# Optimization experiments

Hardware: AMD Instinct MI355X
Metric: run time of the kernel (lower is better)

The kernel has to match this reference:

```python
import jax, jax.numpy as jnp
import numpy as np

DIM = 768
HEADS = 12
HID = 3072  # mlp_ratio * dim
BATCH = 8
FRAMES = 16
GRID = 14
NTOK = GRID * GRID
LN_EPS = 1e-5
EPS = 1e-6


def setup_inputs() -> dict:
    key = jax.random.key(0)
    ks = jax.random.split(key, 8)
    w = lambda k, shape: jax.random.normal(k, shape, jnp.float32) * 0.02
    return {
        "x": jax.random.normal(ks[0], (BATCH * FRAMES, NTOK, DIM), jnp.float32),
        "ln1_w": jnp.ones((DIM,), jnp.float32),
        "ln1_b": jnp.zeros((DIM,), jnp.float32),
        "qkv_w": w(ks[1], (3 * DIM, DIM)),
        "proj_w": w(ks[2], (DIM, DIM)),
        "proj_b": jnp.zeros((DIM,), jnp.float32),
        "ln2_w": jnp.ones((DIM,), jnp.float32),
        "ln2_b": jnp.zeros((DIM,), jnp.float32),
        "fc1_w": w(ks[3], (HID, DIM)),
        "fc1_b": jnp.zeros((HID,), jnp.float32),
        "dw_w": w(ks[4], (HID, 1, 3, 3)),
        "dw_b": jnp.zeros((HID,), jnp.float32),
        "fc2_w": w(ks[5], (DIM, HID)),
        "fc2_b": jnp.zeros((DIM,), jnp.float32),
        "H": GRID,
        "W": GRID,
        "num_frames": FRAMES,
    }


def _layernorm(x, w, b):
    mu = jnp.mean(x, axis=-1, keepdims=True)
    var = jnp.mean(jnp.square(x - mu), axis=-1, keepdims=True)
    return (x - mu) * jax.lax.rsqrt(var + LN_EPS) * w + b


def _joint_ts_attention(xn, qkv_w, proj_w, proj_b, num_frames):
    # xn: (b*f, n, c)
    Bt, n, C = xn.shape
    h = HEADS
    e = C // h
    scale = e ** (-0.5)
    qkv = jnp.einsum('bnc,dc->bnd', xn, qkv_w).reshape(Bt, n, 3, h, e)
    q, k, v = qkv[:, :, 0], qkv[:, :, 1], qkv[:, :, 2]
    # ReLU feature map + scale offset
    q_ = jax.nn.relu(q) + scale
    k_ = jax.nn.relu(k) + scale
    b = Bt // num_frames
    m = num_frames * n  # joint time-space sequence length
    q_ = q_.reshape(b, m, h, e)
    k_ = k_.reshape(b, m, h, e)
    v_ = v.reshape(b, m, h, e)
    # kv_: (b, h, e, e)
    kv = jnp.einsum('bnhe,bnhd->bhed', k_, v_)
    k_sum = jnp.sum(k_, axis=1)  # (b, h, e)
    z = 1.0 / (jnp.einsum('bnhe,bhe->bnh', q_, k_sum) + EPS)  # (b, m, h)
    out = jnp.einsum('bnhe,bhed->bnhd', q_, kv) * z[..., None]  # (b, m, h, e)
    out = out.reshape(Bt, n, C)
    return jnp.einsum('bnc,dc->bnd', out, proj_w) + proj_b


def _dwconv(x, w, b, H, W):
    # x: (B, N, C) -> NCHW depthwise 3x3, pad 1
    Bn, n, c = x.shape
    xi = jnp.transpose(x, (0, 2, 1)).reshape(Bn, c, H, W)
    y = jax.lax.conv_general_dilated(
        xi, w, window_strides=(1, 1), padding=((1, 1), (1, 1)),
        dimension_numbers=('NCHW', 'OIHW', 'NCHW'), feature_group_count=c)
    y = y + b[None, :, None, None]
    return jnp.transpose(y.reshape(Bn, c, n), (0, 2, 1))


def reference(x, ln1_w, ln1_b, qkv_w, proj_w, proj_b, ln2_w, ln2_b,
              fc1_w, fc1_b, dw_w, dw_b, fc2_w, fc2_b, H, W, num_frames):
    # x = x + attn(norm1(x), num_frames)
    x = x + _joint_ts_attention(_layernorm(x, ln1_w, ln1_b), qkv_w, proj_w, proj_b, num_frames)
    # x = x + mlp(norm2(x), H, W)
    xn = _layernorm(x, ln2_w, ln2_b)
    hdn = jnp.einsum('bnc,hc->bnh', xn, fc1_w) + fc1_b
    hdn = _dwconv(hdn, dw_w, dw_b, H, W)
    hdn = jax.nn.gelu(hdn, approximate=False)
    out = jnp.einsum('bnh,ch->bnc', hdn, fc2_w) + fc2_b
    return x + out
```

## Files before the change

kernel.cpp:

```cpp
#include <hip/hip_runtime.h>

typedef unsigned short u16;
typedef unsigned int u32;

typedef __bf16 bf16x8 __attribute__((ext_vector_type(8)));
typedef float f32x4 __attribute__((ext_vector_type(4)));

#define DIM 768
#define HID 3072
#define NTOK 196
#define BT 128
#define NTOKENS (BT * NTOK)
#define MJ 3136
#define HEADS 12

#define QB_ELE ((size_t)NTOKENS * 768)

#define SZ_WB   ((size_t)(2304*768 + 768*768 + 3072*768 + 768*3072) * 2)
#define SZ_XN   ((size_t)NTOKENS * DIM * 2)
#define SZ_QKV  ((size_t)NTOKENS * 2304 * 2)
#define SZ_X2   ((size_t)NTOKENS * DIM * 4)
#define SZ_HDN  ((size_t)NTOKENS * HID * 2)
#define SZ_KV   ((size_t)96 * 4096 * 4)
#define SZ_KS   ((size_t)96 * 64 * 4)
#define WS_NEED (SZ_WB + SZ_XN + SZ_QKV + SZ_X2 + SZ_HDN + SZ_KV + SZ_KS)

static void* g_buf = nullptr;

__device__ __forceinline__ float b2f(u16 u) {
  union { u32 i; float f; } x; x.i = ((u32)u) << 16; return x.f;
}
__device__ __forceinline__ u16 f2b(float f) {
  u32 x = __float_as_uint(f);
  return (u16)((x + 0x7fffu + ((x >> 16) & 1u)) >> 16);
}

__device__ __forceinline__ void gload_lds16(const u16* g, u16* l) {
  __builtin_amdgcn_global_load_lds(
      (const __attribute__((address_space(1))) u32*)g,
      (__attribute__((address_space(3))) u32*)l, 16, 0, 0);
}

__global__ __launch_bounds__(256) void cvt_f32_bf16(const float* __restrict__ in,
    u16* __restrict__ out, int n4)
{
  int i = blockIdx.x * 256 + threadIdx.x;
  if (i < n4) {
    float4 f = ((const float4*)in)[i];
    ushort4 r;
    r.x = f2b(f.x); r.y = f2b(f.y); r.z = f2b(f.z); r.w = f2b(f.w);
    ((ushort4*)out)[i] = r;
  }
}

__global__ __launch_bounds__(256) void zero_f32(float* __restrict__ p, int n) {
  int i = blockIdx.x * 256 + threadIdx.x;
  if (i < n) p[i] = 0.0f;
}

__global__ __launch_bounds__(256) void ln_kernel(const float* __restrict__ xin,
    const float* __restrict__ w, const float* __restrict__ b, u16* __restrict__ out)
{
  const int token = blockIdx.x * 4 + (threadIdx.x >> 6);
  const int lane = threadIdx.x & 63;
  float v[12];
  const float* x = xin + (size_t)token * DIM;
#pragma unroll
  for (int c = 0; c < 3; ++c) {
    float4 f = *(const float4*)(x + c * 256 + lane * 4);
    v[c*4+0] = f.x; v[c*4+1] = f.y; v[c*4+2] = f.z; v[c*4+3] = f.w;
  }
  float s = 0.f, sq = 0.f;
#pragma unroll
  for (int i = 0; i < 12; ++i) { s += v[i]; sq += v[i] * v[i]; }
#pragma unroll
  for (int off = 32; off > 0; off >>= 1) {
    s += __shfl_xor(s, off, 64);
    sq += __shfl_xor(sq, off, 64);
  }
  const float mean = s * (1.0f / 768.0f);
  const float var = sq * (1.0f / 768.0f) - mean * mean;
  const float rstd = rsqrtf(var + 1e-5f);
  u16* o = out + (size_t)token * DIM;
#pragma unroll
  for (int c = 0; c < 3; ++c) {
    float4 wv = *(const float4*)(w + c * 256 + lane * 4);
    float4 bv = *(const float4*)(b + c * 256 + lane * 4);
    ushort4 r;
    r.x = f2b((v[c*4+0] - mean) * rstd * wv.x + bv.x);
    r.y = f2b((v[c*4+1] - mean) * rstd * wv.y + bv.y);
    r.z = f2b((v[c*4+2] - mean) * rstd * wv.z + bv.z);
    r.w = f2b((v[c*4+3] - mean) * rstd * wv.w + bv.w);
    *(ushort4*)(o + c * 256 + lane * 4) = r;
  }
}

template<int MODE, int NXT, int NN, int KK>
__global__ __launch_bounds__(512, 2) void gemm8(
    const u16* __restrict__ A, const u16* __restrict__ W,
    const float* __restrict__ bias, const float* __restrict__ res,
    void* __restrict__ out)
{
  extern __shared__ char smem[];
  u16* As = (u16*)smem;
  u16* Bs = (u16*)(smem + 65536);

  const int t = threadIdx.x;
  const int l = t & 63;
  const int w = t >> 6;
  const int wm = w >> 2;
  const int wn = w & 3;

  constexpr int TOTAL = 98 * NXT;
  constexpr int Q8 = TOTAL >> 3;
  constexpr int R8 = TOTAL & 7;
  const int orig = blockIdx.x;
  const int xcd = orig & 7;
  const int idx = orig >> 3;
  const int wg = (xcd < R8) ? (xcd * (Q8 + 1) + idx)
                            : (R8 * (Q8 + 1) + (xcd - R8) * Q8 + idx);
  const int m0 = (wg / NXT) * 256;
  const int n0 = (wg % NXT) * 256;

  const int srow = w * 16 + (l >> 3);
  const int scol = ((l & 7) ^ (l >> 3)) * 8;
  const u16* gA = A + (size_t)(m0 + srow) * KK + scol;
  const u16* gB = W + (size_t)(n0 + srow) * KK + scol;
  u16* lA = As + w * 1024;
  u16* lB = Bs + w * 1024;

#define STAGE_A(bb, h, kt) do { \
    const u16* g_ = gA + (size_t)(h) * 128 * KK + (size_t)(kt) * 64; \
    u16* l_ = lA + (bb) * 16384 + (h) * 8192; \
    gload_lds16(g_, l_); \
    gload_lds16(g_ + (size_t)8 * KK, l_ + 512); } while (0)
#define STAGE_B(bb, h, kt) do { \
    const u16* g_ = gB + (size_t)(h) * 128 * KK + (size_t)(kt) * 64; \
    u16* l_ = lB + (bb) * 16384 + (h) * 8192; \
    gload_lds16(g_, l_); \
    gload_lds16(g_ + (size_t)8 * KK, l_ + 512); } while (0)

  const int lm = l & 15;
  const int qq = l >> 4;
  const int acol = (qq << 4) ^ ((l & 7) << 4);
  const int abase = (wm * 128 + lm) * 128 + acol;
  const int bbase = (wn * 64 + lm) * 128 + acol;

  f32x4 acc[8][4];
#pragma unroll
  for (int mi = 0; mi < 8; ++mi)
#pragma unroll
    for (int ni = 0; ni < 4; ++ni) acc[mi][ni] = (f32x4){0.f, 0.f, 0.f, 0.f};

  constexpr int NT = KK / 64;

  STAGE_A(0, 0, 0); STAGE_A(0, 1, 0); STAGE_B(0, 0, 0); STAGE_B(0, 1, 0);
  STAGE_A(1, 0, 1); STAGE_A(1, 1, 1);
  asm volatile("s_waitcnt vmcnt(4)" ::: "memory");
  __builtin_amdgcn_s_barrier();

  for (int ti = 0; ti < NT; ++ti) {
    const int cb = ti & 1, nb = cb ^ 1;
    const char* Ac = (const char*)As + cb * 32768;
    const char* Bc = (const char*)Bs + cb * 32768;
    bf16x8 a0[4][2], a1[4][2], b01[2][2], b23[2][2];

#pragma unroll
    for (int mi = 0; mi < 4; ++mi) {
      const int off = abase + mi * 2048;
      a0[mi][0] = *(const bf16x8*)(Ac + off);
      a0[mi][1] = *(const bf16x8*)(Ac + (off ^ 64));
    }
#pragma unroll
    for (int ni = 0; ni < 2; ++ni) {
      const int off = bbase + ni * 2048;
      b01[ni][0] = *(const bf16x8*)(Bc + off);
      b01[ni][1] = *(const bf16x8*)(Bc + (off ^ 64));
    }
    if (ti + 1 < NT) STAGE_B(nb, 0, ti + 1);
    __builtin_amdgcn_s_setprio(1);
#pragma unroll
    for (int mi = 0; mi < 4; ++mi)
#pragma unroll
      for (int ni = 0; ni < 2; ++ni) {
        acc[mi][ni] = __builtin_amdgcn_mfma_f32_16x16x32_bf16(a0[mi][0], b01[ni][0], acc[mi][ni], 0, 0, 0);
        acc[mi][ni] = __builtin_amdgcn_mfma_f32_16x16x32_bf16(a0[mi][1], b01[ni][1], acc[mi][ni], 0, 0, 0);
      }
    __builtin_amdgcn_s_setprio(0);

#pragma unroll
    for (int ni = 0; ni < 2; ++ni) {
      const int off = bbase + (ni + 2) * 2048;
      b23[ni][0] = *(const bf16x8*)(Bc + off);
      b23[ni][1] = *(const bf16x8*)(Bc + (off ^ 64));
    }
    if (ti + 1 < NT) STAGE_B(nb, 1, ti + 1);
    __builtin_amdgcn_s_setprio(1);
#pragma unroll
    for (int mi = 0; mi < 4; ++mi)
#pragma unroll
      for (int ni = 0; ni < 2; ++ni) {
        acc[mi][ni + 2] = __builtin_amdgcn_mfma_f32_16x16x32_bf16(a0[mi][0], b23[ni][0], acc[mi][ni + 2], 0, 0, 0);
        acc[mi][ni + 2] = __builtin_amdgcn_mfma_f32_16x16x32_bf16(a0[mi][1], b23[ni][1], acc[mi][ni + 2], 0, 0, 0);
      }
    __builtin_amdgcn_s_setprio(0);

#pragma unroll
    for (int mi = 0; mi < 4; ++mi) {
      const int off = abase + 8192 + mi * 2048;
      a1[mi][0] = *(const bf16x8*)(Ac + off);
      a1[mi][1] = *(const bf16x8*)(Ac + (off ^ 64));
    }
    __builtin_amdgcn_s_setprio(1);
#pragma unroll
    for (int mi = 0; mi < 4; ++mi)
#pragma unroll
      for (int ni = 0; ni < 2; ++ni) {
        acc[mi + 4][ni + 2] = __builtin_amdgcn_mfma_f32_16x16x32_bf16(a1[mi][0], b23[ni][0], acc[mi + 4][ni + 2], 0, 0, 0);
        acc[mi + 4][ni + 2] = __builtin_amdgcn_mfma_f32_16x16x32_bf16(a1[mi][1], b23[ni][1], acc[mi + 4][ni + 2], 0, 0, 0);
      }
    __builtin_amdgcn_s_setprio(0);

    asm volatile("s_waitcnt lgkmcnt(0)" ::: "memory");
    __builtin_amdgcn_s_barrier();

    if (ti + 2 < NT) { STAGE_A(cb, 0, ti + 2); STAGE_A(cb, 1, ti + 2); }

    __builtin_amdgcn_s_setprio(1);
#pragma unroll
    for (int mi = 0; mi < 4; ++mi)
#pragma unroll
      for (int ni = 0; ni < 2; ++ni) {
        acc[mi + 4][ni] = __builtin_amdgcn_mfma_f32_16x16x32_bf16(a1[mi][0], b01[ni][0], acc[mi + 4][ni], 0, 0, 0);
        acc[mi + 4][ni] = __builtin_amdgcn_mfma_f32_16x16x32_bf16(a1[mi][1], b01[ni][1], acc[mi + 4][ni], 0, 0, 0);
      }
    __builtin_amdgcn_s_setprio(0);

    if (ti + 2 < NT) {
      asm volatile("s_waitcnt vmcnt(4)" ::: "memory");
    } else {
      asm volatile("s_waitcnt vmcnt(0)" ::: "memory");
    }
    __builtin_amdgcn_s_barrier();
  }
#undef STAGE_A
#undef STAGE_B

#pragma unroll
  for (int mi = 0; mi < 8; ++mi) {
    const int rbase = m0 + wm * 128 + mi * 16 + qq * 4;
    const int b = rbase / 3136;
    const int mj = rbase - b * 3136;
#pragma unroll
    for (int ni = 0; ni < 4; ++ni) {
      const int col = n0 + wn * 64 + ni * 16 + lm;
      if (MODE == 0) {
        if (col < 768) {
#pragma unroll
          for (int r = 0; r < 4; ++r) {
            float v = fmaxf(acc[mi][ni][r], 0.0f) + 0.125f;
            ((u16*)out)[(size_t)(rbase + r) * 768 + col] = f2b(v);
          }
        } else {
          const bool isV = (col >= 1536);
          const int cc = col - (isV ? 1536 : 768);
          const int h = cc >> 6, e = cc & 63;
          ushort4 pk;
          float v0 = acc[mi][ni][0], v1 = acc[mi][ni][1];
          float v2 = acc[mi][ni][2], v3 = acc[mi][ni][3];
          if (!isV) {
            v0 = fmaxf(v0, 0.0f) + 0.125f; v1 = fmaxf(v1, 0.0f) + 0.125f;
            v2 = fmaxf(v2, 0.0f) + 0.125f; v3 = fmaxf(v3, 0.0f) + 0.125f;
          }
          pk.x = f2b(v0); pk.y = f2b(v1); pk.z = f2b(v2); pk.w = f2b(v3);
          u16* dst = (u16*)out + (isV ? 2 * QB_ELE : QB_ELE)
                   + ((size_t)((b * 12 + h) * 64 + e)) * 3136 + mj;
          *(ushort4*)dst = pk;
        }
      } else {
        const float bv = bias[col];
#pragma unroll
        for (int r = 0; r < 4; ++r) {
          float v = acc[mi][ni][r];
          const size_t idxo = (size_t)(rbase + r) * NN + col;
          if (MODE == 1) {
            ((float*)out)[idxo] = v + bv + res[idxo];
          } else if (MODE == 2) {
            ((u16*)out)[idxo] = f2b(v + bv);
          } else {
            ((float*)out)[idxo] = v + bv + res[idxo];
          }
        }
      }
    }
  }
}

__global__ __launch_bounds__(256) void ksum_kernel(const u16* __restrict__ KT,
    float* __restrict__ KS)
{
  const int bh = blockIdx.x;
  const int t = threadIdx.x;
  const int w = t >> 6, l = t & 63;
  const u16* base = KT + (size_t)(bh * 64 + w * 16) * 3136;
  for (int r = 0; r < 16; ++r) {
    float s = 0.f;
    const u16* row = base + (size_t)r * 3136;
#pragma unroll
    for (int p = 0; p < 7; ++p) {
      const int m = p * 512 + l * 8;
      if (m < 3136) {
        bf16x8 v = *(const bf16x8*)(row + m);
#pragma unroll
        for (int j = 0; j < 8; ++j) s += (float)v[j];
      }
    }
#pragma unroll
    for (int off = 32; off > 0; off >>= 1) s += __shfl_xor(s, off, 64);
    if (l == 0) KS[bh * 64 + w * 16 + r] = s;
  }
}

__global__ __launch_bounds__(256) void kv_mfma(const u16* __restrict__ KT,
    const u16* __restrict__ VT, float* __restrict__ kv)
{
  const int bh = blockIdx.x;
  const int s = blockIdx.y;
  const int t = threadIdx.x;
  const int l = t & 63, w = t >> 6;
  const int lm = l & 15, qq = l >> 4;
  const size_t mj0 = (size_t)s * 448;
  const u16* ka = KT + (size_t)(bh * 64 + w * 16 + lm) * 3136 + mj0 + qq * 8;
  const u16* vb = VT + (size_t)(bh * 64 + lm) * 3136 + mj0 + qq * 8;

  f32x4 acc[4];
#pragma unroll
  for (int ni = 0; ni < 4; ++ni) acc[ni] = (f32x4){0.f, 0.f, 0.f, 0.f};

#pragma unroll 4
  for (int kk = 0; kk < 14; ++kk) {
    bf16x8 a = *(const bf16x8*)(ka + kk * 32);
#pragma unroll
    for (int ni = 0; ni < 4; ++ni) {
      bf16x8 b = *(const bf16x8*)(vb + (size_t)ni * 16 * 3136 + kk * 32);
      acc[ni] = __builtin_amdgcn_mfma_f32_16x16x32_bf16(a, b, acc[ni], 0, 0, 0);
    }
  }
  float* dst = kv + (size_t)bh * 4096;
#pragma unroll
  for (int ni = 0; ni < 4; ++ni)
#pragma unroll
    for (int r = 0; r < 4; ++r)
      atomicAdd(&dst[(w * 16 + qq * 4 + r) * 64 + ni * 16 + lm], acc[ni][r]);
}

__global__ __launch_bounds__(256) void attn_out(const u16* __restrict__ qb,
    const float* __restrict__ kv, const float* __restrict__ ksum,
    u16* __restrict__ outp)
{
  const int chunk = blockIdx.x;
  const int h = blockIdx.y;
  const int b = blockIdx.z;
  __shared__ float kvs[4096];
  __shared__ float kss[64];
  __shared__ float qs[4096];
  const int t = threadIdx.x;
  const float* kvsrc = kv + (size_t)(b * 12 + h) * 4096;
  for (int i = t; i < 1024; i += 256)
    ((float4*)kvs)[i] = ((const float4*)kvsrc)[i];
  if (t < 64) kss[t] = ksum[(b * 12 + h) * 64 + t];
  __syncthreads();
  const int wv = t >> 6, lane = t & 63;
  float* qw = &qs[wv * 1024];
  const size_t tok0 = (size_t)b * MJ + chunk * 64 + wv * 16;
#pragma unroll
  for (int i = 0; i < 16; ++i) {
    float q = b2f(qb[(tok0 + i) * 768 + h * 64 + lane]);
    float pd = q * kss[lane];
#pragma unroll
    for (int off = 32; off > 0; off >>= 1) pd += __shfl_xor(pd, off, 64);
    qw[i * 64 + lane] = q * (1.0f / (pd + 1e-6f));
  }
  float o[16];
#pragma unroll
  for (int i = 0; i < 16; ++i) o[i] = 0.f;
  for (int e = 0; e < 64; ++e) {
    const float kvc = kvs[e * 64 + lane];
#pragma unroll
    for (int i = 0; i < 16; ++i) o[i] += qw[i * 64 + e] * kvc;
  }
#pragma unroll
  for (int i = 0; i < 16; ++i)
    outp[(tok0 + i) * 768 + h * 64 + lane] = f2b(o[i]);
}

__global__ __launch_bounds__(256) void dwconv_gelu(u16* __restrict__ hdn,
    const float* __restrict__ w, const float* __restrict__ bias)
{
  __shared__ u16 pl[196 * 136];
  const int cb = blockIdx.x;
  const int fr = blockIdx.y;
  const int t = threadIdx.x;
  const int c0 = cb * 128;
  u16* base = hdn + (size_t)fr * 196 * HID + c0;
#pragma unroll
  for (int i = 0; i < 13; ++i) {
    int idx = i * 256 + t;
    if (idx < 3136) {
      int p = idx >> 4, cq = idx & 15;
      *(uint4*)&pl[p * 136 + cq * 8] = *(const uint4*)(base + (size_t)p * HID + cq * 8);
    }
  }
  __syncthreads();
  const int pc = t & 31;
  const int pg = t >> 5;
  const int cc = pc * 4;
  float wr[36];
#pragma unroll
  for (int k = 0; k < 9; ++k)
#pragma unroll
    for (int u = 0; u < 4; ++u) wr[k * 4 + u] = w[(c0 + cc + u) * 9 + k];
  float bv[4];
#pragma unroll
  for (int u = 0; u < 4; ++u) bv[u] = bias[c0 + cc + u];

  for (int j = 0; j < 25; ++j) {
    const int p = pg + j * 8;
    if (p >= 196) break;
    const int py = p / 14, px = p % 14;
    float a0 = bv[0], a1 = bv[1], a2 = bv[2], a3 = bv[3];
#pragma unroll
    for (int ky = 0; ky < 3; ++ky) {
      int yy = py + ky - 1;
      if (yy < 0 || yy > 13) continue;
#pragma unroll
      for (int kx = 0; kx < 3; ++kx) {
        int xx = px + kx - 1;
        if (xx < 0 || xx > 13) continue;
        ushort4 tv = *(const ushort4*)&pl[(yy * 14 + xx) * 136 + cc];
        const float* wk = &wr[(ky * 3 + kx) * 4];
        a0 += wk[0] * b2f(tv.x);
        a1 += wk[1] * b2f(tv.y);
        a2 += wk[2] * b2f(tv.z);
        a3 += wk[3] * b2f(tv.w);
      }
    }
    ushort4 r;
    r.x = f2b(0.5f * a0 * (1.0f + erff(a0 * 0.70710678118654752f)));
    r.y = f2b(0.5f * a1 * (1.0f + erff(a1 * 0.70710678118654752f)));
    r.z = f2b(0.5f * a2 * (1.0f + erff(a2 * 0.70710678118654752f)));
    r.w = f2b(0.5f * a3 * (1.0f + erff(a3 * 0.70710678118654752f)));
    *(ushort4*)(base + (size_t)p * HID + cc) = r;
  }
}

static void set_gemm_attrs() {
  (void)hipFuncSetAttribute(reinterpret_cast<const void*>(&gemm8<0, 9, 2304, 768>),
                            hipFuncAttributeMaxDynamicSharedMemorySize, 131072);
  (void)hipFuncSetAttribute(reinterpret_cast<const void*>(&gemm8<1, 3, 768, 768>),
                            hipFuncAttributeMaxDynamicSharedMemorySize, 131072);
  (void)hipFuncSetAttribute(reinterpret_cast<const void*>(&gemm8<2, 12, 3072, 768>),
                            hipFuncAttributeMaxDynamicSharedMemorySize, 131072);
  (void)hipFuncSetAttribute(reinterpret_cast<const void*>(&gemm8<3, 3, 768, 3072>),
                            hipFuncAttributeMaxDynamicSharedMemorySize, 131072);
}
struct WsInit {
  WsInit() {
    (void)hipMalloc(&g_buf, WS_NEED);
    set_gemm_attrs();
  }
};
static WsInit g_wsinit;

extern "C" void kernel_launch(void* const* d_in, const int* in_sizes, int n_in,
                              void* d_out, int out_size, void* d_ws, size_t ws_size,
                              hipStream_t stream)
{
  (void)in_sizes; (void)n_in; (void)out_size;
  static bool attrs_once = [] { set_gemm_attrs(); return true; }();
  (void)attrs_once;

  const float* x     = (const float*)d_in[0];
  const float* ln1w  = (const float*)d_in[1];
  const float* ln1b  = (const float*)d_in[2];
  const float* qkvw  = (const float*)d_in[3];
  const float* projw = (const float*)d_in[4];
  const float* projb = (const float*)d_in[5];
  const float* ln2w  = (const float*)d_in[6];
  const float* ln2b  = (const float*)d_in[7];
  const float* fc1w  = (const float*)d_in[8];
  const float* fc1b  = (const float*)d_in[9];
  const float* dww   = (const float*)d_in[10];
  const float* dwb   = (const float*)d_in[11];
  const float* fc2w  = (const float*)d_in[12];
  const float* fc2b  = (const float*)d_in[13];

  char* p = (ws_size >= WS_NEED) ? (char*)d_ws : (char*)g_buf;
  u16* WQKV  = (u16*)p;   p += (size_t)2304 * 768 * 2;
  u16* WPROJ = (u16*)p;   p += (size_t)768 * 768 * 2;
  u16* WFC1  = (u16*)p;   p += (size_t)3072 * 768 * 2;
  u16* WFC2  = (u16*)p;   p += (size_t)768 * 3072 * 2;
  u16* XN    = (u16*)p;   p += SZ_XN;
  u16* QKV   = (u16*)p;   p += SZ_QKV;
  float* X2  = (float*)p; p += SZ_X2;
  u16* HDN   = (u16*)p;   p += SZ_HDN;
  float* KV  = (float*)p; p += SZ_KV;
  float* KS  = (float*)p; p += SZ_KS;

  u16* KT = QKV + QB_ELE;
  u16* VT = QKV + 2 * QB_ELE;

  cvt_f32_bf16<<<(2304*768/4 + 255)/256, 256, 0, stream>>>(qkvw, WQKV, 2304*768/4);
  cvt_f32_bf16<<<(768*768/4 + 255)/256, 256, 0, stream>>>(projw, WPROJ, 768*768/4);
  cvt_f32_bf16<<<(3072*768/4 + 255)/256, 256, 0, stream>>>(fc1w, WFC1, 3072*768/4);
  cvt_f32_bf16<<<(768*3072/4 + 255)/256, 256, 0, stream>>>(fc2w, WFC2, 768*3072/4);

  const int nz = 96 * 4096;
  zero_f32<<<(nz + 255) / 256, 256, 0, stream>>>(KV, nz);
  ln_kernel<<<NTOKENS / 4, 256, 0, stream>>>(x, ln1w, ln1b, XN);
  gemm8<0, 9, 2304, 768><<<98 * 9, 512, 131072, stream>>>(XN, WQKV, nullptr, nullptr, QKV);
  ksum_kernel<<<96, 256, 0, stream>>>(KT, KS);
  kv_mfma<<<dim3(96, 7), 256, 0, stream>>>(KT, VT, KV);
  attn_out<<<dim3(49, 12, 8), 256, 0, stream>>>(QKV, KV, KS, XN);
  gemm8<1, 3, 768, 768><<<98 * 3, 512, 131072, stream>>>(XN, WPROJ, projb, x, X2);
  ln_kernel<<<NTOKENS / 4, 256, 0, stream>>>(X2, ln2w, ln2b, QKV);
  gemm8<2, 12, 3072, 768><<<98 * 12, 512, 131072, stream>>>(QKV, WFC1, fc1b, nullptr, HDN);
  dwconv_gelu<<<dim3(24, 128), 256, 0, stream>>>(HDN, dww, dwb);
  gemm8<3, 3, 768, 3072><<<98 * 3, 512, 131072, stream>>>(HDN, WFC2, fc2b, X2, (float*)d_out);
}
```

Baseline: 895.9 us.

## Narrow N-tile for 768-wide GEMMs to fill more CUs; merge weight casts

The GEMM template gains an NF parameter for the N-tile width. The proj and fc2 GEMMs (N=768) now use 192-wide tiles, which gives 392 workgroups instead of 294 so the machine is better filled, and they need less LDS. Staging is reorganized into 64-row chunks so that NF tiles load correctly. The four weight-conversion launches are also merged into one kernel. The narrower tiles reuse each A tile across fewer columns, and the irregular NF=3 path makes register scheduling less uniform.

```diff
diff --git a/kernel.cpp b/kernel.cpp
--- a/kernel.cpp
+++ b/kernel.cpp
@@ -41,16 +41,27 @@
       (__attribute__((address_space(3))) u32*)l, 16, 0, 0);
 }
 
-__global__ __launch_bounds__(256) void cvt_f32_bf16(const float* __restrict__ in,
-    u16* __restrict__ out, int n4)
+#define N4_QKV   442368
+#define N4_PROJ  147456
+#define N4_FC1   589824
+#define N4_FC2   589824
+#define N4_ALL   (N4_QKV + N4_PROJ + N4_FC1 + N4_FC2)
+__global__ __launch_bounds__(256) void cvt_all(const float* __restrict__ a,
+    const float* __restrict__ b, const float* __restrict__ c,
+    const float* __restrict__ d, u16* __restrict__ out)
 {
   int i = blockIdx.x * 256 + threadIdx.x;
-  if (i < n4) {
-    float4 f = ((const float4*)in)[i];
-    ushort4 r;
-    r.x = f2b(f.x); r.y = f2b(f.y); r.z = f2b(f.z); r.w = f2b(f.w);
-    ((ushort4*)out)[i] = r;
-  }
+  if (i >= N4_ALL) return;
+  const float* src;
+  int j = i;
+  if (j < N4_QKV) { src = a; }
+  else if ((j -= N4_QKV) < N4_PROJ) { src = b; }
+  else if ((j -= N4_PROJ) < N4_FC1) { src = c; }
+  else { j -= N4_FC1; src = d; }
+  float4 f = ((const float4*)src)[j];
+  ushort4 r;
+  r.x = f2b(f.x); r.y = f2b(f.y); r.z = f2b(f.z); r.w = f2b(f.w);
+  ((ushort4*)out)[i] = r;
 }
 
 __global__ __launch_bounds__(256) void zero_f32(float* __restrict__ p, int n) {
@@ -95,7 +106,7 @@
   }
 }
 
-template<int MODE, int NXT, int NN, int KK>
+template<int MODE, int NF, int NXT, int NN, int KK>
 __global__ __launch_bounds__(512, 2) void gemm8(
     const u16* __restrict__ A, const u16* __restrict__ W,
     const float* __restrict__ bias, const float* __restrict__ res,
@@ -110,6 +121,7 @@
   const int w = t >> 6;
   const int wm = w >> 2;
   const int wn = w & 3;
+  constexpr int NR = NF - 2;
 
   constexpr int TOTAL = 98 * NXT;
   constexpr int Q8 = TOTAL >> 3;
@@ -120,50 +132,49 @@
   const int wg = (xcd < R8) ? (xcd * (Q8 + 1) + idx)
                             : (R8 * (Q8 + 1) + (xcd - R8) * Q8 + idx);
   const int m0 = (wg / NXT) * 256;
-  const int n0 = (wg % NXT) * 256;
-
-  const int srow = w * 16 + (l >> 3);
+  const int n0 = (wg % NXT) * (NF * 64);
+
   const int scol = ((l & 7) ^ (l >> 3)) * 8;
-  const u16* gA = A + (size_t)(m0 + srow) * KK + scol;
-  const u16* gB = W + (size_t)(n0 + srow) * KK + scol;
-  u16* lA = As + w * 1024;
-  u16* lB = Bs + w * 1024;
-
-#define STAGE_A(bb, h, kt) do { \
-    const u16* g_ = gA + (size_t)(h) * 128 * KK + (size_t)(kt) * 64; \
-    u16* l_ = lA + (bb) * 16384 + (h) * 8192; \
-    gload_lds16(g_, l_); \
-    gload_lds16(g_ + (size_t)8 * KK, l_ + 512); } while (0)
-#define STAGE_B(bb, h, kt) do { \
-    const u16* g_ = gB + (size_t)(h) * 128 * KK + (size_t)(kt) * 64; \
-    u16* l_ = lB + (bb) * 16384 + (h) * 8192; \
-    gload_lds16(g_, l_); \
-    gload_lds16(g_ + (size_t)8 * KK, l_ + 512); } while (0)
+  const u16* gA = A + (size_t)(m0 + w * 8 + (l >> 3)) * KK + scol;
+  const u16* gB = W + (size_t)(n0 + w * 8 + (l >> 3)) * KK + scol;
+  u16* lA = As + w * 512;
+  u16* lB = Bs + w * 512;
+
+#define STAGE_A(bb, u, kt) \
+    gload_lds16(gA + (size_t)(u) * 64 * KK + (size_t)(kt) * 64, \
+                lA + (bb) * 16384 + (u) * 4096)
+#define STAGE_B(bb, u, kt) \
+    gload_lds16(gB + (size_t)(u) * 64 * KK + (size_t)(kt) * 64, \
+                lB + (bb) * NF * 4096 + (u) * 4096)
 
   const int lm = l & 15;
   const int qq = l >> 4;
   const int acol = (qq << 4) ^ ((l & 7) << 4);
   const int abase = (wm * 128 + lm) * 128 + acol;
-  const int bbase = (wn * 64 + lm) * 128 + acol;
-
-  f32x4 acc[8][4];
+  const int bbase = (wn * (NF * 16) + lm) * 128 + acol;
+
+  f32x4 acc[8][NF];
 #pragma unroll
   for (int mi = 0; mi < 8; ++mi)
 #pragma unroll
-    for (int ni = 0; ni < 4; ++ni) acc[mi][ni] = (f32x4){0.f, 0.f, 0.f, 0.f};
+    for (int ni = 0; ni < NF; ++ni) acc[mi][ni] = (f32x4){0.f, 0.f, 0.f, 0.f};
 
   constexpr int NT = KK / 64;
 
-  STAGE_A(0, 0, 0); STAGE_A(0, 1, 0); STAGE_B(0, 0, 0); STAGE_B(0, 1, 0);
-  STAGE_A(1, 0, 1); STAGE_A(1, 1, 1);
+#pragma unroll
+  for (int u = 0; u < 4; ++u) STAGE_A(0, u, 0);
+#pragma unroll
+  for (int u = 0; u < NF; ++u) STAGE_B(0, u, 0);
+#pragma unroll
+  for (int u = 0; u < 4; ++u) STAGE_A(1, u, 1);
   asm volatile("s_waitcnt vmcnt(4)" ::: "memory");
   __builtin_amdgcn_s_barrier();
 
   for (int ti = 0; ti < NT; ++ti) {
     const int cb = ti & 1, nb = cb ^ 1;
     const char* Ac = (const char*)As + cb * 32768;
-    const char* Bc = (const char*)Bs + cb * 32768;
-    bf16x8 a0[4][2], a1[4][2], b01[2][2], b23[2][2];
+    const char* Bc = (const char*)Bs + cb * (NF * 8192);
+    bf16x8 a0[4][2], a1[4][2], b01[2][2], bx[NR][2];
 
 #pragma unroll
     for (int mi = 0; mi < 4; ++mi) {
@@ -177,7 +188,7 @@
       b01[ni][0] = *(const bf16x8*)(Bc + off);
       b01[ni][1] = *(const bf16x8*)(Bc + (off ^ 64));
     }
-    if (ti + 1 < NT) STAGE_B(nb, 0, ti + 1);
+    if (ti + 1 < NT) { STAGE_B(nb, 0, ti + 1); STAGE_B(nb, 1, ti + 1); }
     __builtin_amdgcn_s_setprio(1);
 #pragma unroll
     for (int mi = 0; mi < 4; ++mi)
@@ -189,19 +200,22 @@
     __builtin_amdgcn_s_setprio(0);
 
 #pragma unroll
-    for (int ni = 0; ni < 2; ++ni) {
+    for (int ni = 0; ni < NR; ++ni) {
       const int off = bbase + (ni + 2) * 2048;
-      b23[ni][0] = *(const bf16x8*)(Bc + off);
-      b23[ni][1] = *(const bf16x8*)(Bc + (off ^ 64));
-    }
-    if (ti + 1 < NT) STAGE_B(nb, 1, ti + 1);
+      bx[ni][0] = *(const bf16x8*)(Bc + off);
+      bx[ni][1] = *(const bf16x8*)(Bc + (off ^ 64));
+    }
+    if (ti + 1 < NT) {
+#pragma unroll
+      for (int u = 2; u < NF; ++u) STAGE_B(nb, u, ti + 1);
+    }
     __builtin_amdgcn_s_setprio(1);
 #pragma unroll
     for (int mi = 0; mi < 4; ++mi)
 #pragma unroll
-      for (int ni = 0; ni < 2; ++ni) {
-        acc[mi][ni + 2] = __builtin_amdgcn_mfma_f32_16x16x32_bf16(a0[mi][0], b23[ni][0], acc[mi][ni + 2], 0, 0, 0);
-        acc[mi][ni + 2] = __builtin_amdgcn_mfma_f32_16x16x32_bf16(a0[mi][1], b23[ni][1], acc[mi][ni + 2], 0, 0, 0);
+      for (int ni = 0; ni < NR; ++ni) {
+        acc[mi][ni + 2] = __builtin_amdgcn_mfma_f32_16x16x32_bf16(a0[mi][0], bx[ni][0], acc[mi][ni + 2], 0, 0, 0);
+        acc[mi][ni + 2] = __builtin_amdgcn_mfma_f32_16x16x32_bf16(a0[mi][1], bx[ni][1], acc[mi][ni + 2], 0, 0, 0);
       }
     __builtin_amdgcn_s_setprio(0);
 
@@ -215,16 +229,19 @@
 #pragma unroll
     for (int mi = 0; mi < 4; ++mi)
 #pragma unroll
-      for (int ni = 0; ni < 2; ++ni) {
-        acc[mi + 4][ni + 2] = __builtin_amdgcn_mfma_f32_16x16x32_bf16(a1[mi][0], b23[ni][0], acc[mi + 4][ni + 2], 0, 0, 0);
-        acc[mi + 4][ni + 2] = __builtin_amdgcn_mfma_f32_16x16x32_bf16(a1[mi][1], b23[ni][1], acc[mi + 4][ni + 2], 0, 0, 0);
+      for (int ni = 0; ni < NR; ++ni) {
+        acc[mi + 4][ni + 2] = __builtin_amdgcn_mfma_f32_16x16x32_bf16(a1[mi][0], bx[ni][0], acc[mi + 4][ni + 2], 0, 0, 0);
+        acc[mi + 4][ni + 2] = __builtin_amdgcn_mfma_f32_16x16x32_bf16(a1[mi][1], bx[ni][1], acc[mi + 4][ni + 2], 0, 0, 0);
       }
     __builtin_amdgcn_s_setprio(0);
 
     asm volatile("s_waitcnt lgkmcnt(0)" ::: "memory");
     __builtin_amdgcn_s_barrier();
 
-    if (ti + 2 < NT) { STAGE_A(cb, 0, ti + 2); STAGE_A(cb, 1, ti + 2); }
+    if (ti + 2 < NT) {
+#pragma unroll
+      for (int u = 0; u < 4; ++u) STAGE_A(cb, u, ti + 2);
+    }
 
     __builtin_amdgcn_s_setprio(1);
 #pragma unroll
@@ -252,8 +269,8 @@
     const int b = rbase / 3136;
     const int mj = rbase - b * 3136;
 #pragma unroll
-    for (int ni = 0; ni < 4; ++ni) {
-      const int col = n0 + wn * 64 + ni * 16 + lm;
+    for (int ni = 0; ni < NF; ++ni) {
+      const int col = n0 + wn * (NF * 16) + ni * 16 + lm;
       if (MODE == 0) {
         if (col < 768) {
 #pragma unroll
@@ -455,14 +472,14 @@
 }
 
 static void set_gemm_attrs() {
-  (void)hipFuncSetAttribute(reinterpret_cast<const void*>(&gemm8<0, 9, 2304, 768>),
+  (void)hipFuncSetAttribute(reinterpret_cast<const void*>(&gemm8<0, 4, 9, 2304, 768>),
                             hipFuncAttributeMaxDynamicSharedMemorySize, 131072);
-  (void)hipFuncSetAttribute(reinterpret_cast<const void*>(&gemm8<1, 3, 768, 768>),
+  (void)hipFuncSetAttribute(reinterpret_cast<const void*>(&gemm8<1, 3, 4, 768, 768>),
+                            hipFuncAttributeMaxDynamicSharedMemorySize, 114688);
+  (void)hipFuncSetAttribute(reinterpret_cast<const void*>(&gemm8<2, 4, 12, 3072, 768>),
                             hipFuncAttributeMaxDynamicSharedMemorySize, 131072);
-  (void)hipFuncSetAttribute(reinterpret_cast<const void*>(&gemm8<2, 12, 3072, 768>),
-                            hipFuncAttributeMaxDynamicSharedMemorySize, 131072);
-  (void)hipFuncSetAttribute(reinterpret_cast<const void*>(&gemm8<3, 3, 768, 3072>),
-                            hipFuncAttributeMaxDynamicSharedMemorySize, 131072);
+  (void)hipFuncSetAttribute(reinterpret_cast<const void*>(&gemm8<3, 3, 4, 768, 3072>),
+                            hipFuncAttributeMaxDynamicSharedMemorySize, 114688);
 }
 struct WsInit {
   WsInit() {
@@ -510,21 +527,18 @@
   u16* KT = QKV + QB_ELE;
   u16* VT = QKV + 2 * QB_ELE;
 
-  cvt_f32_bf16<<<(2304*768/4 + 255)/256, 256, 0, stream>>>(qkvw, WQKV, 2304*768/4);
-  cvt_f32_bf16<<<(768*768/4 + 255)/256, 256, 0, stream>>>(projw, WPROJ, 768*768/4);
-  cvt_f32_bf16<<<(3072*768/4 + 255)/256, 256, 0, stream>>>(fc1w, WFC1, 3072*768/4);
-  cvt_f32_bf16<<<(768*3072/4 + 255)/256, 256, 0, stream>>>(fc2w, WFC2, 768*3072/4);
+  cvt_all<<<(N4_ALL + 255) / 256, 256, 0, stream>>>(qkvw, projw, fc1w, fc2w, WQKV);
 
   const int nz = 96 * 4096;
   zero_f32<<<(nz + 255) / 256, 256, 0, stream>>>(KV, nz);
   ln_kernel<<<NTOKENS / 4, 256, 0, stream>>>(x, ln1w, ln1b, XN);
-  gemm8<0, 9, 2304, 768><<<98 * 9, 512, 131072, stream>>>(XN, WQKV, nullptr, nullptr, QKV);
+  gemm8<0, 4, 9, 2304, 768><<<98 * 9, 512, 131072, stream>>>(XN, WQKV, nullptr, nullptr, QKV);
   ksum_kernel<<<96, 256, 0, stream>>>(KT, KS);
   kv_mfma<<<dim3(96, 7), 256, 0, stream>>>(KT, VT, KV);
   attn_out<<<dim3(49, 12, 8), 256, 0, stream>>>(QKV, KV, KS, XN);
-  gemm8<1, 3, 768, 768><<<98 * 3, 512, 131072, stream>>>(XN, WPROJ, projb, x, X2);
+  gemm8<1, 3, 4, 768, 768><<<98 * 4, 512, 114688, stream>>>(XN, WPROJ, projb, x, X2);
   ln_kernel<<<NTOKENS / 4, 256, 0, stream>>>(X2, ln2w, ln2b, QKV);
-  gemm8<2, 12, 3072, 768><<<98 * 12, 512, 131072, stream>>>(QKV, WFC1, fc1b, nullptr, HDN);
+  gemm8<2, 4, 12, 3072, 768><<<98 * 12, 512, 131072, stream>>>(QKV, WFC1, fc1b, nullptr, HDN);
   dwconv_gelu<<<dim3(24, 128), 256, 0, stream>>>(HDN, dww, dwb);
-  gemm8<3, 3, 768, 3072><<<98 * 3, 512, 131072, stream>>>(HDN, WFC2, fc2b, X2, (float*)d_out);
-}
+  gemm8<3, 3, 4, 768, 3072><<<98 * 4, 512, 114688, stream>>>(HDN, WFC2, fc2b, X2, (float*)d_out);
+}
```

New measurement: 909.5 us. Within noise of the previous version (+1.5%).
